# Optimization experiments

Measured on AMD Instinct MI355X. Metric: run time of the kernel, lower is better.

## Reference

```python
import jax, jax.numpy as jnp
import numpy as np

BILATERAL = True
THETA_ALPHA = 8.0   # spatial bandwidth for bilateral term
THETA_BETA = 0.5    # color bandwidth for bilateral term
THETA_GAMMA = 3.0   # spatial bandwidth for spatial-only term


def _features(input_image):
    # input_image: [B, Ci, H, W] -> features [B, N, D]
    B, Ci, H, W = input_image.shape
    N = H * W
    ys, xs = jnp.meshgrid(jnp.arange(H, dtype=jnp.float32),
                          jnp.arange(W, dtype=jnp.float32), indexing='ij')
    pos = jnp.stack([ys, xs], axis=-1).reshape(N, 2)  # [N, 2]
    if BILATERAL:
        sp = jnp.broadcast_to(pos / THETA_ALPHA, (B, N, 2))
        col = input_image.reshape(B, Ci, N).transpose(0, 2, 1) / THETA_BETA  # [B, N, Ci]
        return jnp.concatenate([sp, col], axis=-1)  # [B, N, 2+Ci]
    else:
        return jnp.broadcast_to(pos / THETA_GAMMA, (B, N, 2))


def _gauss_filter(values, feats):
    # values: [B, C, N]; feats: [B, N, D] -> [B, C, N]
    # K_ij = exp(-0.5 * ||f_i - f_j||^2) (unnormalized, as in permutohedral filtering)
    sq = jnp.sum(feats * feats, axis=-1)  # [B, N]
    # squared distances: [B, N, N]
    d2 = sq[:, :, None] + sq[:, None, :] - 2.0 * jnp.einsum('bnd,bmd->bnm', feats, feats)
    K = jnp.exp(-0.5 * jnp.maximum(d2, 0.0))
    return jnp.einsum('bnm,bcm->bcn', K, values)


def setup_inputs() -> dict:
    key = jax.random.key(0)
    k1, k2 = jax.random.split(key)
    cur_state = jax.random.normal(k1, (2, 21, 96, 96), dtype=jnp.float32)
    input_image = jax.random.uniform(k2, (2, 3, 96, 96), dtype=jnp.float32)
    return {"cur_state": cur_state, "input_image": input_image}


def reference(cur_state, input_image):
    assert cur_state.ndim == 4
    B, C, H, W = cur_state.shape
    N = H * W
    feats = _features(input_image)                 # [B, N, D]
    vals = cur_state.reshape(B, C, N)              # [B, C, N]
    out = _gauss_filter(vals, feats)               # [B, C, N]
    return out.reshape(B, C, H, W)
```

## Files before the change

kernel.cpp:

```cpp
#include <hip/hip_runtime.h>
#include <hip/hip_bf16.h>
#include <math.h>


#define HH 96
#define WW 96
#define NN (HH * WW)
#define NB 2
#define NC 21

typedef __attribute__((ext_vector_type(8))) short short8;
typedef __attribute__((ext_vector_type(16))) float f32x16;

constexpr float INV_TA = 0.125f;
constexpr float INV_TB = 2.0f;
constexpr float LOG2E  = 1.44269504088896340736f;

constexpr int BLK    = 256;
constexpr int ITILE  = 64;
constexpr int NIT    = NN / ITILE;
constexpr int G      = 12;
constexpr int NPIECE = 36;
constexpr int NP     = NPIECE / G;

constexpr int VLDS_BYTES = 1024 * 16;
constexpr int SMEM_BYTES = VLDS_BYTES + 512 * 16;

#if defined(__has_builtin)
#if __has_builtin(__builtin_amdgcn_exp2f)
#define EXP2F(x) __builtin_amdgcn_exp2f(x)
#endif
#endif
#ifndef EXP2F
#define EXP2F(x) exp2f(x)
#endif

__device__ __forceinline__ unsigned short bfh(float f) {
    return (unsigned short)((__float_as_uint(f) + 0x8000u) >> 16);
}
__device__ __forceinline__ float bff(unsigned short u) {
    return __uint_as_float(((unsigned)u) << 16);
}
__device__ __forceinline__ unsigned pk2(float a, float b) {
    const unsigned u0 = __float_as_uint(a) + 0x8000u;
    const unsigned u1 = __float_as_uint(b) + 0x8000u;
    return __builtin_amdgcn_perm(u1, u0, 0x07060302u);
}

__global__ __launch_bounds__(BLK)
void perm_gauss_fused(const float* __restrict__ cur,
                      const float* __restrict__ img,
                      float* __restrict__ out) {
    __shared__ __align__(16) unsigned char smem[SMEM_BYTES];
    uint4* vlds = (uint4*)smem;
    uint4* flds = (uint4*)(smem + VLDS_BYTES);

    const int tid  = threadIdx.x;
    const int lane = tid & 63;
    const int wave = tid >> 6;
    const int isub = wave & 1;
    const int jh   = wave >> 1;
    const int il   = lane & 31;
    const int half = lane >> 5;

    const int it = blockIdx.x, g = blockIdx.y, b = blockIdx.z;
    const int ibase = it * ITILE;
    const float* curb = cur + (size_t)b * NC * NN;
    const float* imgb = img + (size_t)b * 3 * NN;
    float* outb = out + (size_t)b * NC * NN;
    const unsigned short one = 0x3F80;

    const int ig = ibase + isub * 32 + il;
    const float yi = (float)(ig / WW) * INV_TA;
    const float xi = (float)(ig % WW) * INV_TA;
    unsigned short chi[3], cli[3]; float cfi[3];
    #pragma unroll
    for (int d = 0; d < 3; ++d) {
        const float c = imgb[d * NN + ig] * INV_TB;
        chi[d] = bfh(c);
        const float chf = bff(chi[d]);
        cli[d] = bfh(c - chf);
        cfi[d] = chf + bff(cli[d]);
    }
    const float ei = -0.5f * (yi * yi + xi * xi +
                              cfi[0] * cfi[0] + cfi[1] * cfi[1] + cfi[2] * cfi[2]);
    const unsigned short eih = bfh(ei);
    const unsigned short eil = bfh(ei - bff(eih));
    union { unsigned short u[8]; short8 v; } bfi;
    if (half == 0) {
        bfi.u[0] = bfh(yi); bfi.u[1] = bfh(xi);
        bfi.u[2] = chi[0]; bfi.u[3] = chi[1]; bfi.u[4] = chi[2];
        bfi.u[5] = chi[0]; bfi.u[6] = chi[1]; bfi.u[7] = chi[2];
    } else {
        bfi.u[0] = cli[0]; bfi.u[1] = cli[1]; bfi.u[2] = cli[2];
        bfi.u[3] = one; bfi.u[4] = one; bfi.u[5] = eih; bfi.u[6] = eil;
        bfi.u[7] = 0;
    }

    f32x16 acc0, acc1, zz;
    #pragma unroll
    for (int r = 0; r < 16; ++r) { acc0[r] = 0.0f; acc1[r] = 0.0f; zz[r] = 0.0f; }

    for (int p = 0; p < NP; ++p) {
        const int pidx = g * NP + p;
        const int j0 = pidx * 256;
        __syncthreads();

        {
            const int g32 = tid & 31;
            const int jb = j0 + (g32 >> 2) * 32 + ((g32 >> 1) & 1) * 16 + (g32 & 1) * 4;
            const int slotb = g32 * 32;
            const int sw = g32 & 7;
            #pragma unroll
            for (int it4 = 0; it4 < 4; ++it4) {
                const int c = it4 * 8 + (tid >> 5);
                float4 qa = {0, 0, 0, 0}, qb = {0, 0, 0, 0};
                if (c < NC) {
                    const float* row = curb + (size_t)c * NN;
                    qa = *(const float4*)(row + jb);
                    qb = *(const float4*)(row + jb + 8);
                }
                uint4 o;
                o.x = pk2(qa.x, qa.y); o.y = pk2(qa.z, qa.w);
                o.z = pk2(qb.x, qb.y); o.w = pk2(qb.z, qb.w);
                vlds[slotb + (c ^ sw)] = o;
            }
        }
        {
            const int j = j0 + tid;
            const float y = (float)(j / WW) * INV_TA;
            const float x = (float)(j % WW) * INV_TA;
            unsigned short ch[3], cl[3]; float cf[3];
            #pragma unroll
            for (int d = 0; d < 3; ++d) {
                const float c = imgb[d * NN + j] * INV_TB;
                ch[d] = bfh(c);
                const float chf = bff(ch[d]);
                cl[d] = bfh(c - chf);
                cf[d] = chf + bff(cl[d]);
            }
            const float e = -0.5f * (y * y + x * x +
                                     cf[0] * cf[0] + cf[1] * cf[1] + cf[2] * cf[2]);
            const unsigned short eh = bfh(e);
            const unsigned short el = bfh(e - bff(eh));
            union { unsigned short u[8]; uint4 q; } f0, f1;
            f0.u[0] = bfh(y); f0.u[1] = bfh(x);
            f0.u[2] = ch[0]; f0.u[3] = ch[1]; f0.u[4] = ch[2];
            f0.u[5] = cl[0]; f0.u[6] = cl[1]; f0.u[7] = cl[2];
            f1.u[0] = ch[0]; f1.u[1] = ch[1]; f1.u[2] = ch[2];
            f1.u[3] = eh; f1.u[4] = el; f1.u[5] = one; f1.u[6] = one;
            f1.u[7] = 0;
            flds[tid] = f0.q;
            flds[256 + tid] = f1.q;
        }
        __syncthreads();

        #pragma unroll
        for (int q = 0; q < 4; ++q) {
            const int jbl = jh * 4 + q;
            const short8 afj = *(const short8*)&flds[half * 256 + jbl * 32 + il];
            const f32x16 s =
                __builtin_amdgcn_mfma_f32_32x32x16_bf16(afj, bfi.v, zz, 0, 0, 0);
            float w[16];
            #pragma unroll
            for (int r = 0; r < 16; ++r) w[r] = EXP2F(s[r] * LOG2E);
            union { unsigned dw[4]; short8 v; } a1, a2;
            #pragma unroll
            for (int d = 0; d < 4; ++d) {
                a1.dw[d] = pk2(w[2 * d],     w[2 * d + 1]);
                a2.dw[d] = pk2(w[8 + 2 * d], w[9 + 2 * d]);
            }
            const int gA = 4 * jbl + half;
            const int gB = 4 * jbl + 2 + half;
            const short8 v1 = *(const short8*)&vlds[gA * 32 + (il ^ (gA & 7))];
            const short8 v2 = *(const short8*)&vlds[gB * 32 + (il ^ (gB & 7))];
            f32x16& A = (q & 1) ? acc1 : acc0;
            A = __builtin_amdgcn_mfma_f32_32x32x16_bf16(a1.v, v1, A, 0, 0, 0);
            A = __builtin_amdgcn_mfma_f32_32x32x16_bf16(a2.v, v2, A, 0, 0, 0);
        }
    }

    #pragma unroll
    for (int r = 0; r < 16; ++r) acc0[r] += acc1[r];

    __syncthreads();
    float* mytile = (float*)smem + wave * 32 * 33;
    #pragma unroll
    for (int r = 0; r < 16; ++r) {
        const int row = (r & 3) + 8 * (r >> 2) + 4 * half;
        mytile[row * 33 + il] = acc0[r];
    }
    __builtin_amdgcn_s_waitcnt(0);
    #pragma unroll
    for (int cc = 0; cc < 11; ++cc) {
        const int c = 2 * cc + half;
        if (c < NC) {
            const float v = mytile[il * 33 + c];
            atomicAdd(&outb[(size_t)c * NN + ibase + isub * 32 + il], v);
        }
    }
}

extern "C" void kernel_launch(void* const* d_in, const int* in_sizes, int n_in,
                              void* d_out, int out_size, void* d_ws, size_t ws_size,
                              hipStream_t stream) {
    const float* cur = (const float*)d_in[0];
    const float* img = (const float*)d_in[1];
    float* out = (float*)d_out;

    dim3 grid(NIT, G, NB);
    perm_gauss_fused<<<grid, BLK, 0, stream>>>(cur, img, out);
}
```

Baseline: 108.5 us.

## Precompute bf16 values and features once in a prep kernel before the MFMA pass

Adds a prep kernel that converts cur_state to packed bf16 tiles and builds the hi/lo bf16 feature vectors once per call, writing both to the workspace. The main kernel then copies value tiles straight into LDS and reads feature fragments directly from global memory, instead of every block redoing the conversion and feature maths for each piece. This removes the conversion work repeated across the many i-tiles. It also uses the hardware packed bf16 convert when available and a two-wide multiply before exp2. The cost is an extra kernel launch and a workspace round-trip through L2.

```diff
diff --git a/kernel.cpp b/kernel.cpp
--- a/kernel.cpp
+++ b/kernel.cpp
@@ -11,6 +11,7 @@
 
 typedef __attribute__((ext_vector_type(8))) short short8;
 typedef __attribute__((ext_vector_type(16))) float f32x16;
+typedef __attribute__((ext_vector_type(2))) float float2v;
 
 constexpr float INV_TA = 0.125f;
 constexpr float INV_TB = 2.0f;
@@ -23,13 +24,22 @@
 constexpr int NPIECE = 36;
 constexpr int NP     = NPIECE / G;
 
-constexpr int VLDS_BYTES = 1024 * 16;
-constexpr int SMEM_BYTES = VLDS_BYTES + 512 * 16;
+constexpr size_t VG_BYTES = (size_t)NB * NPIECE * 1024 * 16;
+constexpr size_t FJA_OFF  = VG_BYTES;
+
+constexpr int SMEM_BYTES = 4 * 32 * 33 * 4;
+
+constexpr int NVU  = NB * NPIECE * 1024;
+constexpr int NFT  = NB * NN;
+constexpr int PREP_TASKS = NVU + NFT;
 
 #if defined(__has_builtin)
 #if __has_builtin(__builtin_amdgcn_exp2f)
 #define EXP2F(x) __builtin_amdgcn_exp2f(x)
 #endif
+#if __has_builtin(__builtin_amdgcn_cvt_pk_bf16_f32)
+#define HAS_CVT_PK_BF16 1
+#endif
 #endif
 #ifndef EXP2F
 #define EXP2F(x) exp2f(x)
@@ -41,19 +51,81 @@
 __device__ __forceinline__ float bff(unsigned short u) {
     return __uint_as_float(((unsigned)u) << 16);
 }
-__device__ __forceinline__ unsigned pk2(float a, float b) {
+__device__ __forceinline__ unsigned pack2bf(float a, float b) {
+#ifdef HAS_CVT_PK_BF16
+    auto t = __builtin_amdgcn_cvt_pk_bf16_f32(a, b);
+    unsigned r; __builtin_memcpy(&r, &t, 4); return r;
+#else
     const unsigned u0 = __float_as_uint(a) + 0x8000u;
     const unsigned u1 = __float_as_uint(b) + 0x8000u;
     return __builtin_amdgcn_perm(u1, u0, 0x07060302u);
+#endif
 }
 
 __global__ __launch_bounds__(BLK)
-void perm_gauss_fused(const float* __restrict__ cur,
-                      const float* __restrict__ img,
-                      float* __restrict__ out) {
+void prep_kernel(const float* __restrict__ cur, const float* __restrict__ img,
+                 unsigned char* __restrict__ ws) {
+    const int t = blockIdx.x * BLK + threadIdx.x;
+    if (t < NVU) {
+        const int b  = t / (NPIECE * 1024);
+        const int r  = t % (NPIECE * 1024);
+        const int rr = r & 1023;
+        const int piece = r >> 10;
+        const int jbl = rr >> 7;
+        const int m   = (rr >> 6) & 1;
+        const int h   = (rr >> 5) & 1;
+        const int c   = rr & 31;
+        const int jb = piece * 256 + jbl * 32 + m * 16 + 4 * h;
+        float4 qa = {0, 0, 0, 0}, qb = {0, 0, 0, 0};
+        if (c < NC) {
+            const float* row = cur + ((size_t)b * NC + c) * NN;
+            qa = *(const float4*)(row + jb);
+            qb = *(const float4*)(row + jb + 8);
+        }
+        uint4 o;
+        o.x = pack2bf(qa.x, qa.y); o.y = pack2bf(qa.z, qa.w);
+        o.z = pack2bf(qb.x, qb.y); o.w = pack2bf(qb.z, qb.w);
+        *(uint4*)(ws + (size_t)t * 16) = o;
+    } else {
+        const int tf = t - NVU;
+        const int b = tf / NN;
+        const int j = tf % NN;
+        const float y = (float)(j / WW) * INV_TA;
+        const float x = (float)(j % WW) * INV_TA;
+        const float* ib = img + (size_t)b * 3 * NN;
+        unsigned short ch[3], cl[3]; float cf[3];
+        #pragma unroll
+        for (int d = 0; d < 3; ++d) {
+            const float c = ib[d * NN + j] * INV_TB;
+            ch[d] = bfh(c);
+            const float chf = bff(ch[d]);
+            cl[d] = bfh(c - chf);
+            cf[d] = chf + bff(cl[d]);
+        }
+        const float e = -0.5f * (y * y + x * x +
+                                 cf[0] * cf[0] + cf[1] * cf[1] + cf[2] * cf[2]);
+        const unsigned short eh = bfh(e);
+        const unsigned short el = bfh(e - bff(eh));
+        const unsigned short one = 0x3F80;
+        const int piece = j >> 8, jl = j & 255;
+        unsigned short* u0 = (unsigned short*)
+            (ws + FJA_OFF + ((((size_t)b * NPIECE + piece) * 2 + 0) * 256 + jl) * 16);
+        unsigned short* u1 = (unsigned short*)
+            (ws + FJA_OFF + ((((size_t)b * NPIECE + piece) * 2 + 1) * 256 + jl) * 16);
+        u0[0] = bfh(y); u0[1] = bfh(x);
+        u0[2] = ch[0]; u0[3] = ch[1]; u0[4] = ch[2];
+        u0[5] = cl[0]; u0[6] = cl[1]; u0[7] = cl[2];
+        u1[0] = ch[0]; u1[1] = ch[1]; u1[2] = ch[2]; u1[3] = eh; u1[4] = el;
+        u1[5] = one; u1[6] = one; u1[7] = 0;
+    }
+}
+
+__global__ __launch_bounds__(BLK)
+void perm_gauss_mfma(const float* __restrict__ img,
+                     const unsigned char* __restrict__ ws,
+                     float* __restrict__ out) {
     __shared__ __align__(16) unsigned char smem[SMEM_BYTES];
     uint4* vlds = (uint4*)smem;
-    uint4* flds = (uint4*)(smem + VLDS_BYTES);
 
     const int tid  = threadIdx.x;
     const int lane = tid & 63;
@@ -65,7 +137,6 @@
 
     const int it = blockIdx.x, g = blockIdx.y, b = blockIdx.z;
     const int ibase = it * ITILE;
-    const float* curb = cur + (size_t)b * NC * NN;
     const float* imgb = img + (size_t)b * 3 * NN;
     float* outb = out + (size_t)b * NC * NN;
     const unsigned short one = 0x3F80;
@@ -101,85 +172,48 @@
     #pragma unroll
     for (int r = 0; r < 16; ++r) { acc0[r] = 0.0f; acc1[r] = 0.0f; zz[r] = 0.0f; }
 
+    const float2v lg2 = {LOG2E, LOG2E};
+
     for (int p = 0; p < NP; ++p) {
         const int pidx = g * NP + p;
-        const int j0 = pidx * 256;
         __syncthreads();
-
-        {
-            const int g32 = tid & 31;
-            const int jb = j0 + (g32 >> 2) * 32 + ((g32 >> 1) & 1) * 16 + (g32 & 1) * 4;
-            const int slotb = g32 * 32;
-            const int sw = g32 & 7;
-            #pragma unroll
-            for (int it4 = 0; it4 < 4; ++it4) {
-                const int c = it4 * 8 + (tid >> 5);
-                float4 qa = {0, 0, 0, 0}, qb = {0, 0, 0, 0};
-                if (c < NC) {
-                    const float* row = curb + (size_t)c * NN;
-                    qa = *(const float4*)(row + jb);
-                    qb = *(const float4*)(row + jb + 8);
-                }
-                uint4 o;
-                o.x = pk2(qa.x, qa.y); o.y = pk2(qa.z, qa.w);
-                o.z = pk2(qb.x, qb.y); o.w = pk2(qb.z, qb.w);
-                vlds[slotb + (c ^ sw)] = o;
-            }
-        }
-        {
-            const int j = j0 + tid;
-            const float y = (float)(j / WW) * INV_TA;
-            const float x = (float)(j % WW) * INV_TA;
-            unsigned short ch[3], cl[3]; float cf[3];
-            #pragma unroll
-            for (int d = 0; d < 3; ++d) {
-                const float c = imgb[d * NN + j] * INV_TB;
-                ch[d] = bfh(c);
-                const float chf = bff(ch[d]);
-                cl[d] = bfh(c - chf);
-                cf[d] = chf + bff(cl[d]);
-            }
-            const float e = -0.5f * (y * y + x * x +
-                                     cf[0] * cf[0] + cf[1] * cf[1] + cf[2] * cf[2]);
-            const unsigned short eh = bfh(e);
-            const unsigned short el = bfh(e - bff(eh));
-            union { unsigned short u[8]; uint4 q; } f0, f1;
-            f0.u[0] = bfh(y); f0.u[1] = bfh(x);
-            f0.u[2] = ch[0]; f0.u[3] = ch[1]; f0.u[4] = ch[2];
-            f0.u[5] = cl[0]; f0.u[6] = cl[1]; f0.u[7] = cl[2];
-            f1.u[0] = ch[0]; f1.u[1] = ch[1]; f1.u[2] = ch[2];
-            f1.u[3] = eh; f1.u[4] = el; f1.u[5] = one; f1.u[6] = one;
-            f1.u[7] = 0;
-            flds[tid] = f0.q;
-            flds[256 + tid] = f1.q;
-        }
+        const uint4* vsrc = (const uint4*)(ws + ((size_t)b * NPIECE + pidx) * 16384);
+        #pragma unroll
+        for (int k = 0; k < 4; ++k) vlds[k * 256 + tid] = vsrc[k * 256 + tid];
         __syncthreads();
+
+        const uint4* fws = (const uint4*)
+            (ws + FJA_OFF + ((size_t)b * NPIECE + pidx) * 8192);
 
         #pragma unroll
         for (int q = 0; q < 4; ++q) {
             const int jbl = jh * 4 + q;
-            const short8 afj = *(const short8*)&flds[half * 256 + jbl * 32 + il];
+            short8 afj;
+            { uint4 t = fws[half * 256 + jbl * 32 + il];
+              __builtin_memcpy(&afj, &t, 16); }
             const f32x16 s =
                 __builtin_amdgcn_mfma_f32_32x32x16_bf16(afj, bfi.v, zz, 0, 0, 0);
+            union { f32x16 v; float2v p[8]; } su; su.v = s;
             float w[16];
             #pragma unroll
-            for (int r = 0; r < 16; ++r) w[r] = EXP2F(s[r] * LOG2E);
+            for (int d8 = 0; d8 < 8; ++d8) {
+                const float2v a = su.p[d8] * lg2;
+                w[2 * d8]     = EXP2F(a.x);
+                w[2 * d8 + 1] = EXP2F(a.y);
+            }
             union { unsigned dw[4]; short8 v; } a1, a2;
             #pragma unroll
             for (int d = 0; d < 4; ++d) {
-                a1.dw[d] = pk2(w[2 * d],     w[2 * d + 1]);
-                a2.dw[d] = pk2(w[8 + 2 * d], w[9 + 2 * d]);
+                a1.dw[d] = pack2bf(w[2 * d],     w[2 * d + 1]);
+                a2.dw[d] = pack2bf(w[8 + 2 * d], w[9 + 2 * d]);
             }
-            const int gA = 4 * jbl + half;
-            const int gB = 4 * jbl + 2 + half;
-            const short8 v1 = *(const short8*)&vlds[gA * 32 + (il ^ (gA & 7))];
-            const short8 v2 = *(const short8*)&vlds[gB * 32 + (il ^ (gB & 7))];
+            const short8 v1 = *(const short8*)&vlds[(4 * jbl + half) * 32 + il];
+            const short8 v2 = *(const short8*)&vlds[(4 * jbl + 2 + half) * 32 + il];
             f32x16& A = (q & 1) ? acc1 : acc0;
             A = __builtin_amdgcn_mfma_f32_32x32x16_bf16(a1.v, v1, A, 0, 0, 0);
             A = __builtin_amdgcn_mfma_f32_32x32x16_bf16(a2.v, v2, A, 0, 0, 0);
         }
     }
-
     #pragma unroll
     for (int r = 0; r < 16; ++r) acc0[r] += acc1[r];
 
@@ -190,7 +224,6 @@
         const int row = (r & 3) + 8 * (r >> 2) + 4 * half;
         mytile[row * 33 + il] = acc0[r];
     }
-    __builtin_amdgcn_s_waitcnt(0);
     #pragma unroll
     for (int cc = 0; cc < 11; ++cc) {
         const int c = 2 * cc + half;
@@ -207,7 +240,9 @@
     const float* cur = (const float*)d_in[0];
     const float* img = (const float*)d_in[1];
     float* out = (float*)d_out;
-
+    unsigned char* ws = (unsigned char*)d_ws;
+
+    prep_kernel<<<PREP_TASKS / BLK, BLK, 0, stream>>>(cur, img, ws);
     dim3 grid(NIT, G, NB);
-    perm_gauss_fused<<<grid, BLK, 0, stream>>>(cur, img, out);
-}
+    perm_gauss_mfma<<<grid, BLK, 0, stream>>>(img, ws, out);
+}
```

After: 98.12 us. 9.6% less time.
